# Kernel tuning notes

Hardware: AMD Instinct MI355X
Metric: run time of the kernel (lower is better)

The kernel has to match this reference:

```python
import jax, jax.numpy as jnp
import numpy as np

N_NODES = 50000
N_EDGES = 800000
IN_CH = 128
EDGE_DIM = 16
HID = 64
HEADS = 2
OUT = 64


def _transformer_conv(x, src, dst, edge_attr, Wq, bq, Wk, bk, Wv, bv, We, Ws, bs, H, C):
    # PyG TransformerConv, eval mode, concat=True, root_weight=True, beta=False.
    N = x.shape[0]
    q = (x @ Wq + bq).reshape(N, H, C)
    k = (x @ Wk + bk).reshape(N, H, C)
    v = (x @ Wv + bv).reshape(N, H, C)
    e = (edge_attr @ We).reshape(-1, H, C)          # [E,H,C], lin_edge has no bias
    kj = k[src] + e                                  # gather + edge-aware key
    vj = v[src] + e                                  # gather + edge-aware value
    alpha = jnp.einsum('ehc,ehc->eh', q[dst], kj) / jnp.sqrt(jnp.asarray(C, x.dtype))
    # segment softmax over incoming edges of each target node
    m = jax.ops.segment_max(alpha, dst, num_segments=N)
    m = jnp.where(jnp.isfinite(m), m, jnp.zeros_like(m))
    ex = jnp.exp(alpha - m[dst])
    den = jax.ops.segment_sum(ex, dst, num_segments=N)
    a = ex / (den[dst] + 1e-16)                      # [E,H]
    agg = jax.ops.segment_sum(a[:, :, None] * vj, dst, num_segments=N)  # [N,H,C]
    return agg.reshape(N, H * C) + (x @ Ws + bs)     # concat heads + root skip


def setup_inputs() -> dict:
    key = jax.random.key(0)
    ks = jax.random.split(key, 24)
    s = 0.05
    d1 = HEADS * HID   # 128
    d2 = 1 * OUT       # 64
    inp = {
        'x': jax.random.normal(ks[0], (N_NODES, IN_CH), jnp.float32),
        'edge_index': jax.random.randint(ks[1], (2, N_EDGES), 0, N_NODES, jnp.int32),
        'edge_attr': jax.random.normal(ks[2], (N_EDGES, EDGE_DIM), jnp.float32),
        # layer 1 params
        'Wq1': jax.random.normal(ks[3], (IN_CH, d1), jnp.float32) * s,
        'bq1': jnp.zeros((d1,), jnp.float32),
        'Wk1': jax.random.normal(ks[4], (IN_CH, d1), jnp.float32) * s,
        'bk1': jnp.zeros((d1,), jnp.float32),
        'Wv1': jax.random.normal(ks[5], (IN_CH, d1), jnp.float32) * s,
        'bv1': jnp.zeros((d1,), jnp.float32),
        'We1': jax.random.normal(ks[6], (EDGE_DIM, d1), jnp.float32) * s,
        'Ws1': jax.random.normal(ks[7], (IN_CH, d1), jnp.float32) * s,
        'bs1': jnp.zeros((d1,), jnp.float32),
        # layer 2 params (heads=1)
        'Wq2': jax.random.normal(ks[8], (d1, d2), jnp.float32) * s,
        'bq2': jnp.zeros((d2,), jnp.float32),
        'Wk2': jax.random.normal(ks[9], (d1, d2), jnp.float32) * s,
        'bk2': jnp.zeros((d2,), jnp.float32),
        'Wv2': jax.random.normal(ks[10], (d1, d2), jnp.float32) * s,
        'bv2': jnp.zeros((d2,), jnp.float32),
        'We2': jax.random.normal(ks[11], (EDGE_DIM, d2), jnp.float32) * s,
        'Ws2': jax.random.normal(ks[12], (d1, d2), jnp.float32) * s,
        'bs2': jnp.zeros((d2,), jnp.float32),
    }
    return inp


def reference(x, edge_index, edge_attr,
              Wq1, bq1, Wk1, bk1, Wv1, bv1, We1, Ws1, bs1,
              Wq2, bq2, Wk2, bk2, Wv2, bv2, We2, Ws2, bs2):
    src, dst = edge_index[0], edge_index[1]
    h = _transformer_conv(x, src, dst, edge_attr,
                          Wq1, bq1, Wk1, bk1, Wv1, bv1, We1, Ws1, bs1, HEADS, HID)
    h = jax.nn.relu(h)
    out = _transformer_conv(h, src, dst, edge_attr,
                            Wq2, bq2, Wk2, bk2, Wv2, bv2, We2, Ws2, bs2, 1, OUT)
    return out
```

## Files before the change

### kernel.cpp

```cpp
#include <hip/hip_runtime.h>
#include <hip/hip_bf16.h>

#define NN 50000
#define NE 800000
#define NBKT 196
#define EPB 4096
#define NCB 196

#define PB_BH   NCB
#define PB_PW1  (PB_BH + 32)
#define PB_PW2  (PB_PW1 + 16)
#define PB_PA1  (PB_PW2 + 2)
#define PB_PA2  (PB_PA1 + 1)

#define DB_BKT  NBKT
#define DB_ALL  (DB_BKT + 3125)

typedef __attribute__((ext_vector_type(8))) short bf16x8;
typedef __attribute__((ext_vector_type(4))) float f32x4;

__device__ __forceinline__ float2 bfp(uint32_t u) {
    union { uint32_t i; float f; } lo, hi;
    lo.i = u << 16;
    hi.i = u & 0xffff0000u;
    return make_float2(lo.f, hi.f);
}
__device__ __forceinline__ float bf1(uint16_t u) {
    union { uint32_t i; float f; } x; x.i = ((uint32_t)u) << 16; return x.f;
}
__device__ __forceinline__ float4 bfp4(uint32_t a, uint32_t b) {
    const float2 lo = bfp(a), hi = bfp(b);
    return make_float4(lo.x, lo.y, hi.x, hi.y);
}

template<int M>
__device__ __forceinline__ void pack_w_dev(
    int t, const float* __restrict__ Wq, const float* __restrict__ Wk,
    const float* __restrict__ Wv, const float* __restrict__ Wsk,
    const float* __restrict__ bq, const float* __restrict__ bk,
    const float* __restrict__ bv, const float* __restrict__ bsk,
    __hip_bfloat16* __restrict__ Wp, float* __restrict__ bcat)
{
    constexpr int NFQ = M / 16;
    constexpr int NF_TOT = 4 * NFQ;
    if (t >= 4 * NF_TOT * 64) return;
    const int l  = t & 63;
    const int fg = (t >> 6) % NF_TOT;
    const int s  = t / (64 * NF_TOT);
    const int sec = fg / NFQ;
    const int fl  = fg % NFQ;
    const float* W = sec == 0 ? Wq : sec == 1 ? Wk : sec == 2 ? Wv : Wsk;
    const int col = fl * 16 + (l & 15);
    const int k0  = s * 32 + (l >> 4) * 8;
    __hip_bfloat16 tmp[8];
    #pragma unroll
    for (int j = 0; j < 8; ++j) tmp[j] = __float2bfloat16(W[(size_t)(k0 + j) * M + col]);
    *reinterpret_cast<uint4*>(Wp + ((size_t)(fg * 4 + s) * 64 + l) * 8) =
        *reinterpret_cast<const uint4*>(tmp);
    if (s == 0 && (l >> 4) == 0) {
        const float* B = sec == 0 ? bq : sec == 1 ? bk : sec == 2 ? bv : bsk;
        bcat[fg * 16 + (l & 15)] = B[col];
    }
}

template<int MW, int MO>
__device__ __forceinline__ void pack_wq_dev(
    int t, const float* __restrict__ Wq, const float* __restrict__ We,
    const float* __restrict__ bq,
    __hip_bfloat16* __restrict__ Ap, float* __restrict__ B0)
{
    constexpr int NF = MO / 16;
    if (t >= 4 * NF * 64) return;
    const int l  = t & 63;
    const int fg = (t >> 6) % NF;
    const int s  = t / (64 * NF);
    const int col = fg * 16 + (l & 15);
    const int h = col >> 4;
    const int r = col & 15;
    const int k0 = s * 32 + (l >> 4) * 8;
    __hip_bfloat16 tmp[8];
    #pragma unroll
    for (int jj = 0; jj < 8; ++jj) {
        float acc = 0.f;
        for (int c = 0; c < 64; ++c)
            acc += Wq[(size_t)(k0 + jj) * MW + h * 64 + c] * We[r * MW + h * 64 + c];
        tmp[jj] = __float2bfloat16(acc * 0.125f);
    }
    *reinterpret_cast<uint4*>(Ap + ((size_t)(fg * 4 + s) * 64 + l) * 8) =
        *reinterpret_cast<const uint4*>(tmp);
    if (s == 0 && (l >> 4) == 0) {
        float acc = 0.f;
        for (int c = 0; c < 64; ++c) acc += bq[h * 64 + c] * We[r * MW + h * 64 + c];
        B0[col] = acc * 0.125f;
    }
}

__global__ __launch_bounds__(256)
void prep(const int* __restrict__ dstp, int* __restrict__ blkcnt,
          const float* Wq1, const float* Wk1, const float* Wv1, const float* Ws1,
          const float* bq1, const float* bk1, const float* bv1, const float* bs1,
          const float* We1,
          const float* Wq2, const float* Wk2, const float* Wv2, const float* Ws2,
          const float* bq2, const float* bk2, const float* bv2, const float* bs2,
          const float* We2,
          __hip_bfloat16* Wp1, float* bcat1,
          __hip_bfloat16* Wp2, float* bcat2)
{
    const int b = blockIdx.x;
    const int t = threadIdx.x;
    if (b < PB_BH) {
        __shared__ int bins[NBKT];
        if (t < NBKT) bins[t] = 0;
        __syncthreads();
        const int e0 = b * EPB;
        const int nedge = min(EPB, NE - e0);
        for (int j = 0; j < EPB / 256; ++j) {
            const int idx = t + j * 256;
            if (idx < nedge) atomicAdd(&bins[dstp[e0 + idx] >> 8], 1);
        }
        __syncthreads();
        if (t < NBKT) blkcnt[b * NBKT + t] = bins[t];
    } else if (b < PB_PW1) {
        pack_w_dev<128>((b - PB_BH) * 256 + t, Wq1, Wk1, Wv1, Ws1,
                        bq1, bk1, bv1, bs1, Wp1, bcat1);
    } else if (b < PB_PW2) {
        pack_w_dev<64>((b - PB_PW1) * 256 + t, Wq2, Wk2, Wv2, Ws2,
                       bq2, bk2, bv2, bs2, Wp2, bcat2);
    } else if (b < PB_PA1) {
        pack_wq_dev<128, 32>((b - PB_PW2) * 256 + t, Wq1, We1, bq1,
                             Wp1 + (size_t)32 * 2048, bcat1 + 512);
    } else {
        pack_wq_dev<64, 16>((b - PB_PA1) * 256 + t, Wq2, We2, bq2,
                            Wp2 + (size_t)16 * 2048, bcat2 + 256);
    }
}

__global__ __launch_bounds__(256)
void passC(const int* __restrict__ dstp, const int* __restrict__ srcp,
           const int* __restrict__ blkcnt, int2* __restrict__ ebuf,
           int* __restrict__ bucket_start)
{
    __shared__ int gbase[NBKT];
    __shared__ int lofs0[NBKT];
    __shared__ int lcur[NBKT];
    __shared__ int stmp[256];
    __shared__ int2 buf[EPB];

    const int blk = blockIdx.x;
    const int t = threadIdx.x;

    int partial = 0, total = 0;
    if (t < NBKT) {
        for (int b = 0; b < NCB; ++b) {
            const int v = blkcnt[b * NBKT + t];
            partial += (b < blk) ? v : 0;
            total += v;
        }
    }
    stmp[t] = (t < NBKT) ? total : 0;
    __syncthreads();
    #pragma unroll
    for (int d = 1; d < 256; d <<= 1) {
        const int v = (t >= d) ? stmp[t - d] : 0;
        __syncthreads();
        stmp[t] += v;
        __syncthreads();
    }
    const int bstart = stmp[t] - ((t < NBKT) ? total : 0);
    if (t < NBKT) gbase[t] = bstart + partial;
    if (blk == 0 && t < NBKT) bucket_start[t] = bstart;
    if (blk == 0 && t == NBKT - 1) bucket_start[NBKT] = stmp[t];

    if (t < NBKT) lcur[t] = 0;
    __syncthreads();
    const int e0 = blk * EPB;
    const int nedge = min(EPB, NE - e0);
    for (int j = 0; j < EPB / 256; ++j) {
        const int idx = t + j * 256;
        if (idx < nedge) atomicAdd(&lcur[dstp[e0 + idx] >> 8], 1);
    }
    __syncthreads();
    stmp[t] = (t < NBKT) ? lcur[t] : 0;
    __syncthreads();
    const int own = stmp[t];
    #pragma unroll
    for (int d = 1; d < 256; d <<= 1) {
        const int v = (t >= d) ? stmp[t - d] : 0;
        __syncthreads();
        stmp[t] += v;
        __syncthreads();
    }
    if (t < NBKT) { lofs0[t] = stmp[t] - own; lcur[t] = stmp[t] - own; }
    __syncthreads();

    for (int j = 0; j < EPB / 256; ++j) {
        const int idx = t + j * 256;
        if (idx < nedge) {
            const int e = e0 + idx;
            const int d_ = dstp[e];
            const int bkt = d_ >> 8;
            const int q = atomicAdd(&lcur[bkt], 1);
            buf[q] = make_int2(srcp[e] | ((d_ & 255) << 16), e | (bkt << 20));
        }
    }
    __syncthreads();

    for (int j = 0; j < EPB / 256; ++j) {
        const int q = t + j * 256;
        if (q < nedge) {
            const int2 v = buf[q];
            const int bkt = v.y >> 20;
            ebuf[gbase[bkt] + (q - lofs0[bkt])] = v;
        }
    }
}

template<int M, int MO, bool F32IN>
__device__ __forceinline__
void gemm_dev(int blk, int tid, const void* __restrict__ xin,
              const __hip_bfloat16* __restrict__ Wp,
              const float* __restrict__ bcat,
              __hip_bfloat16* __restrict__ q, __hip_bfloat16* __restrict__ kv,
              __hip_bfloat16* __restrict__ skip, float* __restrict__ wqo)
{
    constexpr int NF_TOT = (4 * M + MO) / 16;
    constexpr int NFW = (NF_TOT + 3) / 4;
    const int wid  = tid >> 6;
    const int l    = tid & 63;
    const int row0 = blk * 16;
    const int rowg = row0 + (l & 15);
    const int kb   = l >> 4;

    f32x4 acc[NFW];
    #pragma unroll
    for (int f = 0; f < NFW; ++f) acc[f] = f32x4{0.f, 0.f, 0.f, 0.f};

    const bf16x8* wp8 = reinterpret_cast<const bf16x8*>(Wp);
    #pragma unroll
    for (int s = 0; s < 4; ++s) {
        bf16x8 a;
        if constexpr (F32IN) {
            const float* xf = (const float*)xin;
            const float4 a0 = *reinterpret_cast<const float4*>(
                xf + (size_t)rowg * 128 + s * 32 + kb * 8);
            const float4 a1 = *reinterpret_cast<const float4*>(
                xf + (size_t)rowg * 128 + s * 32 + kb * 8 + 4);
            union { __hip_bfloat16 h[8]; bf16x8 v; } u;
            u.h[0] = __float2bfloat16(a0.x); u.h[1] = __float2bfloat16(a0.y);
            u.h[2] = __float2bfloat16(a0.z); u.h[3] = __float2bfloat16(a0.w);
            u.h[4] = __float2bfloat16(a1.x); u.h[5] = __float2bfloat16(a1.y);
            u.h[6] = __float2bfloat16(a1.z); u.h[7] = __float2bfloat16(a1.w);
            a = u.v;
        } else {
            const __hip_bfloat16* xb = (const __hip_bfloat16*)xin;
            a = *reinterpret_cast<const bf16x8*>(xb + (size_t)rowg * 128 + s * 32 + kb * 8);
        }
        #pragma unroll
        for (int f = 0; f < NFW; ++f) {
            const int fg = wid + 4 * f;
            if (fg < NF_TOT)
                acc[f] = __builtin_amdgcn_mfma_f32_16x16x32_bf16(
                    a, wp8[(size_t)(fg * 4 + s) * 64 + l], acc[f], 0, 0, 0);
        }
    }

    const int cl = l & 15;
    #pragma unroll
    for (int f = 0; f < NFW; ++f) {
        const int fg = wid + 4 * f;
        if (fg >= NF_TOT) continue;
        const int cg = fg * 16 + cl;
        const float bb = bcat[cg];
        #pragma unroll
        for (int j = 0; j < 4; ++j) {
            const int row = row0 + kb * 4 + j;
            const float val = acc[f][j] + bb;
            if (cg < M) {
                q[(size_t)row * M + cg] = __float2bfloat16(val * 0.125f);
            } else if (cg < 2 * M) {
                const int c = cg - M;
                kv[(size_t)row * 2 * M + (c >> 2) * 8 + (c & 3)] = __float2bfloat16(val);
            } else if (cg < 3 * M) {
                const int c = cg - 2 * M;
                kv[(size_t)row * 2 * M + (c >> 2) * 8 + 4 + (c & 3)] = __float2bfloat16(val);
            } else if (cg < 4 * M) {
                skip[(size_t)row * M + (cg - 3 * M)] = __float2bfloat16(val);
            } else {
                wqo[(size_t)row * MO + (cg - 4 * M)] = val;
            }
        }
    }
}

template<int M, int MO, bool F32IN>
__global__ __launch_bounds__(256)
void gemm_fused(const void* __restrict__ xin,
                const __hip_bfloat16* __restrict__ Wp,
                const float* __restrict__ bcat,
                __hip_bfloat16* __restrict__ q, __hip_bfloat16* __restrict__ kv,
                __hip_bfloat16* __restrict__ skip, float* __restrict__ wqo)
{
    gemm_dev<M, MO, F32IN>(blockIdx.x, threadIdx.x, xin, Wp, bcat, q, kv, skip, wqo);
}

__global__ __launch_bounds__(256)
void passD_mid(const int2* __restrict__ ebuf, const int* __restrict__ bucket_start,
               const float* __restrict__ ea,
               int* __restrict__ off, int* __restrict__ srcs,
               __hip_bfloat16* __restrict__ eap,
               const float* __restrict__ x, const __hip_bfloat16* __restrict__ Wp1,
               const float* __restrict__ bcat1, __hip_bfloat16* __restrict__ q1b,
               __hip_bfloat16* __restrict__ kv1, __hip_bfloat16* __restrict__ sk1b,
               float* __restrict__ wq1)
{
    __shared__ int nbins[256];
    __shared__ int ncur[256];
    __shared__ int stmp[256];

    if (blockIdx.x >= DB_BKT) {
        gemm_dev<128, 32, true>(blockIdx.x - DB_BKT, threadIdx.x, x, Wp1, bcat1,
                                q1b, kv1, sk1b, wq1);
        return;
    }

    const int b = blockIdx.x;
    const int t = threadIdx.x;
    const int bs = bucket_start[b];
    const int be = bucket_start[b + 1];

    nbins[t] = 0;
    __syncthreads();
    for (int i = bs + t; i < be; i += 256)
        atomicAdd(&nbins[(ebuf[i].x >> 16) & 255], 1);
    __syncthreads();

    const int own = nbins[t];
    stmp[t] = own;
    __syncthreads();
    #pragma unroll
    for (int d = 1; d < 256; d <<= 1) {
        const int v = (t >= d) ? stmp[t - d] : 0;
        __syncthreads();
        stmp[t] += v;
        __syncthreads();
    }
    const int excl = stmp[t] - own;
    ncur[t] = excl;
    const int node = b * 256 + t;
    if (node <= NN) off[node] = bs + excl;
    __syncthreads();

    for (int i = bs + t; i < be; i += 256) {
        const int2 v = ebuf[i];
        const int dl = (v.x >> 16) & 255;
        const int p = bs + atomicAdd(&ncur[dl], 1);
        const int srcn = v.x & 0xffff;
        const int e = v.y & 0xfffff;
        srcs[p] = srcn;
        const float4* ea4 = reinterpret_cast<const float4*>(ea) + (size_t)e * 4;
        const float4 a0 = ea4[0], a1 = ea4[1], a2 = ea4[2], a3 = ea4[3];
        const float af[16] = {a0.x,a0.y,a0.z,a0.w, a1.x,a1.y,a1.z,a1.w,
                              a2.x,a2.y,a2.z,a2.w, a3.x,a3.y,a3.z,a3.w};
        __hip_bfloat16 tmp[16];
        #pragma unroll
        for (int r = 0; r < 16; ++r) tmp[r] = __float2bfloat16(af[r]);
        uint4* dp = reinterpret_cast<uint4*>(eap + (size_t)p * 16);
        dp[0] = *reinterpret_cast<const uint4*>(&tmp[0]);
        dp[1] = *reinterpret_cast<const uint4*>(&tmp[8]);
    }
}

__global__ __launch_bounds__(256)
void agg_l1(const int* __restrict__ off, const int* __restrict__ srcs,
            const __hip_bfloat16* __restrict__ eap,
            const float* __restrict__ We,
            const float* __restrict__ wq,
            const __hip_bfloat16* __restrict__ qb,
            const __hip_bfloat16* __restrict__ kv,
            const __hip_bfloat16* __restrict__ skb,
            __hip_bfloat16* __restrict__ hb)
{
    __shared__ float wes[16 * 128];
    for (int i = threadIdx.x; i < 16 * 128; i += 256) wes[i] = We[i];
    __syncthreads();

    const int node = blockIdx.x * 4 + (threadIdx.x >> 6);
    const int lane = threadIdx.x & 63;
    const int hf   = lane >> 5;
    const int hl   = lane & 31;
    const int g    = lane & 15;
    const int ch   = hl * 4;

    const size_t nb = (size_t)node * 128;
    const uint16_t* qu = reinterpret_cast<const uint16_t*>(qb);
    const uint2 qw = *reinterpret_cast<const uint2*>(qu + nb + ch);
    const float4 qv = bfp4(qw.x, qw.y);
    const float wqv = wq[(size_t)node * 32 + (hl >> 4) * 16 + g];
    const uint16_t* kvu = reinterpret_cast<const uint16_t*>(kv);
    const uint16_t* eau = reinterpret_cast<const uint16_t*>(eap);

    float acc0 = 0.f, acc1 = 0.f, acc2 = 0.f, acc3 = 0.f, den = 0.f, eacc = 0.f;
    const int beg = off[node], end = off[node + 1];

    for (int i = beg; i < end; i += 8) {
        const int ii0 = i + hf,     ii1 = i + 2 + hf;
        const int ii2 = i + 4 + hf, ii3 = i + 6 + hf;
        const bool v0 = ii0 < end, v1 = ii1 < end, v2 = ii2 < end, v3 = ii3 < end;
        const int i0 = v0 ? ii0 : beg, i1 = v1 ? ii1 : beg;
        const int i2 = v2 ? ii2 : beg, i3 = v3 ? ii3 : beg;
        const int s0 = srcs[i0], s1 = srcs[i1], s2 = srcs[i2], s3 = srcs[i3];
        const uint4 x0 = *reinterpret_cast<const uint4*>(kvu + (size_t)s0 * 256 + hl * 8);
        const uint4 x1 = *reinterpret_cast<const uint4*>(kvu + (size_t)s1 * 256 + hl * 8);
        const uint4 x2 = *reinterpret_cast<const uint4*>(kvu + (size_t)s2 * 256 + hl * 8);
        const uint4 x3 = *reinterpret_cast<const uint4*>(kvu + (size_t)s3 * 256 + hl * 8);
        const float ea0 = bf1(eau[(size_t)i0 * 16 + g]);
        const float ea1 = bf1(eau[(size_t)i1 * 16 + g]);
        const float ea2 = bf1(eau[(size_t)i2 * 16 + g]);
        const float ea3 = bf1(eau[(size_t)i3 * 16 + g]);
        const float4 k0 = bfp4(x0.x, x0.y), k1 = bfp4(x1.x, x1.y);
        const float4 k2 = bfp4(x2.x, x2.y), k3 = bfp4(x3.x, x3.y);
        float p0 = fmaf(qv.x, k0.x, fmaf(qv.y, k0.y,
                   fmaf(qv.z, k0.z, fmaf(qv.w, k0.w, ea0 * wqv))));
        float p1 = fmaf(qv.x, k1.x, fmaf(qv.y, k1.y,
                   fmaf(qv.z, k1.z, fmaf(qv.w, k1.w, ea1 * wqv))));
        float p2 = fmaf(qv.x, k2.x, fmaf(qv.y, k2.y,
                   fmaf(qv.z, k2.z, fmaf(qv.w, k2.w, ea2 * wqv))));
        float p3 = fmaf(qv.x, k3.x, fmaf(qv.y, k3.y,
                   fmaf(qv.z, k3.z, fmaf(qv.w, k3.w, ea3 * wqv))));
        #pragma unroll
        for (int m = 1; m < 16; m <<= 1) {
            p0 += __shfl_xor(p0, m, 64);
            p1 += __shfl_xor(p1, m, 64);
            p2 += __shfl_xor(p2, m, 64);
            p3 += __shfl_xor(p3, m, 64);
        }
        const float ex0 = v0 ? __expf(p0) : 0.f;
        const float ex1 = v1 ? __expf(p1) : 0.f;
        const float ex2 = v2 ? __expf(p2) : 0.f;
        const float ex3 = v3 ? __expf(p3) : 0.f;
        const float4 w0 = bfp4(x0.z, x0.w), w1 = bfp4(x1.z, x1.w);
        const float4 w2 = bfp4(x2.z, x2.w), w3 = bfp4(x3.z, x3.w);
        acc0 = fmaf(ex0, w0.x, fmaf(ex1, w1.x, fmaf(ex2, w2.x, fmaf(ex3, w3.x, acc0))));
        acc1 = fmaf(ex0, w0.y, fmaf(ex1, w1.y, fmaf(ex2, w2.y, fmaf(ex3, w3.y, acc1))));
        acc2 = fmaf(ex0, w0.z, fmaf(ex1, w1.z, fmaf(ex2, w2.z, fmaf(ex3, w3.z, acc2))));
        acc3 = fmaf(ex0, w0.w, fmaf(ex1, w1.w, fmaf(ex2, w2.w, fmaf(ex3, w3.w, acc3))));
        den += (ex0 + ex1) + (ex2 + ex3);
        eacc = fmaf(ex0, ea0, fmaf(ex1, ea1, fmaf(ex2, ea2, fmaf(ex3, ea3, eacc))));
    }

    acc0 += __shfl_xor(acc0, 32, 64);
    acc1 += __shfl_xor(acc1, 32, 64);
    acc2 += __shfl_xor(acc2, 32, 64);
    acc3 += __shfl_xor(acc3, 32, 64);
    den  += __shfl_xor(den, 32, 64);
    eacc += __shfl_xor(eacc, 32, 64);

    const int gb = lane & 16;
    #pragma unroll
    for (int r = 0; r < 16; ++r) {
        const float er = __shfl(eacc, gb + r, 64);
        const float4 w = *reinterpret_cast<const float4*>(&wes[r * 128 + ch]);
        acc0 = fmaf(er, w.x, acc0);
        acc1 = fmaf(er, w.y, acc1);
        acc2 = fmaf(er, w.z, acc2);
        acc3 = fmaf(er, w.w, acc3);
    }

    if (hf == 0) {
        const float inv = 1.f / (den + 1e-16f);
        const uint16_t* sku = reinterpret_cast<const uint16_t*>(skb);
        const uint2 skw = *reinterpret_cast<const uint2*>(sku + nb + ch);
        const float4 sk = bfp4(skw.x, skw.y);
        __hip_bfloat16 hp[4] = {
            __float2bfloat16(fmaxf(fmaf(acc0, inv, sk.x), 0.f)),
            __float2bfloat16(fmaxf(fmaf(acc1, inv, sk.y), 0.f)),
            __float2bfloat16(fmaxf(fmaf(acc2, inv, sk.z), 0.f)),
            __float2bfloat16(fmaxf(fmaf(acc3, inv, sk.w), 0.f))};
        *reinterpret_cast<uint2*>(hb + nb + ch) = *reinterpret_cast<const uint2*>(hp);
    }
}

__global__ __launch_bounds__(256)
void agg_l2(const int* __restrict__ off, const int* __restrict__ srcs,
            const __hip_bfloat16* __restrict__ eap,
            const float* __restrict__ We,
            const float* __restrict__ wq,
            const __hip_bfloat16* __restrict__ qb,
            const __hip_bfloat16* __restrict__ kv,
            const __hip_bfloat16* __restrict__ skb,
            float* __restrict__ out)
{
    __shared__ float wes[16 * 64];
    for (int i = threadIdx.x; i < 16 * 64; i += 256) wes[i] = We[i];
    __syncthreads();

    const int node = blockIdx.x * 4 + (threadIdx.x >> 6);
    const int lane = threadIdx.x & 63;
    const int grp  = lane >> 4;
    const int g    = lane & 15;
    const int ch   = g * 4;

    const size_t nb = (size_t)node * 64;
    const uint16_t* qu = reinterpret_cast<const uint16_t*>(qb);
    const uint2 qw = *reinterpret_cast<const uint2*>(qu + nb + ch);
    const float4 qv = bfp4(qw.x, qw.y);
    const float wqv = wq[(size_t)node * 16 + g];
    const uint16_t* kvu = reinterpret_cast<const uint16_t*>(kv);
    const uint16_t* eau = reinterpret_cast<const uint16_t*>(eap);

    float acc0 = 0.f, acc1 = 0.f, acc2 = 0.f, acc3 = 0.f, den = 0.f, eacc = 0.f;
    const int beg = off[node], end = off[node + 1];

    for (int i = beg; i < end; i += 8) {
        const int ii0 = i + grp, ii1 = i + 4 + grp;
        const bool v0 = ii0 < end, v1 = ii1 < end;
        const int i0 = v0 ? ii0 : beg, i1 = v1 ? ii1 : beg;
        const int s0 = srcs[i0], s1 = srcs[i1];
        const uint4 x0 = *reinterpret_cast<const uint4*>(kvu + (size_t)s0 * 128 + g * 8);
        const uint4 x1 = *reinterpret_cast<const uint4*>(kvu + (size_t)s1 * 128 + g * 8);
        const float ea0 = bf1(eau[(size_t)i0 * 16 + g]);
        const float ea1 = bf1(eau[(size_t)i1 * 16 + g]);
        const float4 k0 = bfp4(x0.x, x0.y), k1 = bfp4(x1.x, x1.y);
        float p0 = fmaf(qv.x, k0.x, fmaf(qv.y, k0.y,
                   fmaf(qv.z, k0.z, fmaf(qv.w, k0.w, ea0 * wqv))));
        float p1 = fmaf(qv.x, k1.x, fmaf(qv.y, k1.y,
                   fmaf(qv.z, k1.z, fmaf(qv.w, k1.w, ea1 * wqv))));
        #pragma unroll
        for (int m = 1; m < 16; m <<= 1) {
            p0 += __shfl_xor(p0, m, 64);
            p1 += __shfl_xor(p1, m, 64);
        }
        const float ex0 = v0 ? __expf(p0) : 0.f;
        const float ex1 = v1 ? __expf(p1) : 0.f;
        const float4 w0 = bfp4(x0.z, x0.w), w1 = bfp4(x1.z, x1.w);
        acc0 = fmaf(ex0, w0.x, fmaf(ex1, w1.x, acc0));
        acc1 = fmaf(ex0, w0.y, fmaf(ex1, w1.y, acc1));
        acc2 = fmaf(ex0, w0.z, fmaf(ex1, w1.z, acc2));
        acc3 = fmaf(ex0, w0.w, fmaf(ex1, w1.w, acc3));
        den += ex0 + ex1;
        eacc = fmaf(ex0, ea0, fmaf(ex1, ea1, eacc));
    }

    acc0 += __shfl_xor(acc0, 16, 64);  acc0 += __shfl_xor(acc0, 32, 64);
    acc1 += __shfl_xor(acc1, 16, 64);  acc1 += __shfl_xor(acc1, 32, 64);
    acc2 += __shfl_xor(acc2, 16, 64);  acc2 += __shfl_xor(acc2, 32, 64);
    acc3 += __shfl_xor(acc3, 16, 64);  acc3 += __shfl_xor(acc3, 32, 64);
    den  += __shfl_xor(den, 16, 64);   den  += __shfl_xor(den, 32, 64);
    eacc += __shfl_xor(eacc, 16, 64);  eacc += __shfl_xor(eacc, 32, 64);

    #pragma unroll
    for (int r = 0; r < 16; ++r) {
        const float er = __shfl(eacc, r, 64);
        const float4 w = *reinterpret_cast<const float4*>(&wes[r * 64 + ch]);
        acc0 = fmaf(er, w.x, acc0);
        acc1 = fmaf(er, w.y, acc1);
        acc2 = fmaf(er, w.z, acc2);
        acc3 = fmaf(er, w.w, acc3);
    }

    if (lane < 16) {
        const float inv = 1.f / (den + 1e-16f);
        const uint16_t* sku = reinterpret_cast<const uint16_t*>(skb);
        const uint2 skw = *reinterpret_cast<const uint2*>(sku + nb + ch);
        const float4 sk = bfp4(skw.x, skw.y);
        *reinterpret_cast<float4*>(out + nb + ch) =
            make_float4(fmaf(acc0, inv, sk.x), fmaf(acc1, inv, sk.y),
                        fmaf(acc2, inv, sk.z), fmaf(acc3, inv, sk.w));
    }
}

extern "C" void kernel_launch(void* const* d_in, const int* in_sizes, int n_in,
                              void* d_out, int out_size, void* d_ws, size_t ws_size,
                              hipStream_t stream) {
    const float* x     = (const float*)d_in[0];
    const int*   ei    = (const int*)  d_in[1];
    const float* eattr = (const float*)d_in[2];
    const float* Wq1 = (const float*)d_in[3],  *bq1 = (const float*)d_in[4];
    const float* Wk1 = (const float*)d_in[5],  *bk1 = (const float*)d_in[6];
    const float* Wv1 = (const float*)d_in[7],  *bv1 = (const float*)d_in[8];
    const float* We1 = (const float*)d_in[9];
    const float* Ws1 = (const float*)d_in[10], *bs1 = (const float*)d_in[11];
    const float* Wq2 = (const float*)d_in[12], *bq2 = (const float*)d_in[13];
    const float* Wk2 = (const float*)d_in[14], *bk2 = (const float*)d_in[15];
    const float* Wv2 = (const float*)d_in[16], *bv2 = (const float*)d_in[17];
    const float* We2 = (const float*)d_in[18];
    const float* Ws2 = (const float*)d_in[19], *bs2 = (const float*)d_in[20];

    const int* srcp = ei;
    const int* dstp = ei + NE;

    char* base = (char*)d_ws;
    size_t o = 0;
    auto alloc = [&](size_t bytes) -> void* {
        void* p = base + o;
        o = (o + bytes + 511) & ~(size_t)511;
        return p;
    };
    float* wq1   = (float*)alloc((size_t)NN * 32 * 4);
    float* wq2   = (float*)alloc((size_t)NN * 16 * 4);
    float* bcat1 = (float*)alloc(544 * 4);
    float* bcat2 = (float*)alloc(272 * 4);
    int*  blkcnt = (int*)alloc((size_t)NCB * NBKT * 4);
    int2* ebuf   = (int2*)alloc((size_t)NE * 8);
    int*  bstart = (int*)alloc((NBKT + 1) * 4);
    int*  srcs   = (int*)alloc((size_t)NE * 4);
    int*  off    = (int*)alloc((size_t)(NN + 1) * 4);
    __hip_bfloat16* eap  = (__hip_bfloat16*)alloc((size_t)NE * 16 * 2);
    __hip_bfloat16* q1b  = (__hip_bfloat16*)alloc((size_t)NN * 128 * 2);
    __hip_bfloat16* sk1b = (__hip_bfloat16*)alloc((size_t)NN * 128 * 2);
    __hip_bfloat16* hb   = (__hip_bfloat16*)alloc((size_t)NN * 128 * 2);
    __hip_bfloat16* kv1  = (__hip_bfloat16*)alloc((size_t)NN * 256 * 2);
    __hip_bfloat16* Wp1  = (__hip_bfloat16*)alloc((size_t)34 * 2048 * 2);
    __hip_bfloat16* Wp2  = (__hip_bfloat16*)alloc((size_t)17 * 2048 * 2);
    __hip_bfloat16* q2b  = q1b;
    __hip_bfloat16* sk2b = sk1b;
    __hip_bfloat16* kv2  = kv1;

    prep<<<PB_PA2, 256, 0, stream>>>(dstp, blkcnt,
        Wq1, Wk1, Wv1, Ws1, bq1, bk1, bv1, bs1, We1,
        Wq2, Wk2, Wv2, Ws2, bq2, bk2, bv2, bs2, We2,
        Wp1, bcat1, Wp2, bcat2);

    passC<<<NCB, 256, 0, stream>>>(dstp, srcp, blkcnt, ebuf, bstart);

    passD_mid<<<DB_ALL, 256, 0, stream>>>(ebuf, bstart, eattr, off, srcs, eap,
                                          x, Wp1, bcat1, q1b, kv1, sk1b, wq1);

    agg_l1<<<NN / 4, 256, 0, stream>>>(off, srcs, eap, We1, wq1, q1b, kv1, sk1b, hb);

    gemm_fused<64, 16, false><<<NN / 16, 256, 0, stream>>>(
        hb, Wp2, bcat2, q2b, kv2, sk2b, wq2);

    agg_l2<<<NN / 4, 256, 0, stream>>>(off, srcs, eap, We2, wq2, q2b, kv2, sk2b, (float*)d_out);
}
```

Before: 259.7 us.

## Move edge-attr bf16 conversion into bucket scatter and widen blocks to 1024 threads

The bucket scatter pass now scatters each edge straight to its global slot with shared atomics, dropping the shared-memory staging and local prefix scan. It also converts edge attributes to bf16 and writes them to an intermediate array at bucket position. The per-node sort pass then copies 32-byte bf16 rows instead of re-reading 64-byte fp32 rows at random edge indices. Both passes switch to 1024-thread blocks, and the fused GEMM blocks each handle four 16-row tiles. The direct global scatter loses write coalescing and adds a 25.6MB intermediate buffer plus an extra copy.

```diff
diff --git a/kernel.cpp b/kernel.cpp
--- a/kernel.cpp
+++ b/kernel.cpp
@@ -14,7 +14,8 @@
 #define PB_PA2  (PB_PA1 + 1)
 
 #define DB_BKT  NBKT
-#define DB_ALL  (DB_BKT + 3125)
+#define DB_GT   782
+#define DB_ALL  (DB_BKT + DB_GT)
 
 typedef __attribute__((ext_vector_type(8))) short bf16x8;
 typedef __attribute__((ext_vector_type(4))) float f32x4;
@@ -135,16 +136,14 @@
     }
 }
 
-__global__ __launch_bounds__(256)
+__global__ __launch_bounds__(1024)
 void passC(const int* __restrict__ dstp, const int* __restrict__ srcp,
-           const int* __restrict__ blkcnt, int2* __restrict__ ebuf,
+           const float* __restrict__ ea, const int* __restrict__ blkcnt,
+           uint32_t* __restrict__ sidx, __hip_bfloat16* __restrict__ eap1,
            int* __restrict__ bucket_start)
 {
-    __shared__ int gbase[NBKT];
-    __shared__ int lofs0[NBKT];
-    __shared__ int lcur[NBKT];
+    __shared__ int gcur[NBKT];
     __shared__ int stmp[256];
-    __shared__ int2 buf[EPB];
 
     const int blk = blockIdx.x;
     const int t = threadIdx.x;
@@ -157,60 +156,44 @@
             total += v;
         }
     }
-    stmp[t] = (t < NBKT) ? total : 0;
-    __syncthreads();
-    #pragma unroll
+    if (t < 256) stmp[t] = (t < NBKT) ? total : 0;
+    __syncthreads();
     for (int d = 1; d < 256; d <<= 1) {
-        const int v = (t >= d) ? stmp[t - d] : 0;
+        const int v = (t < 256 && t >= d) ? stmp[t - d] : 0;
         __syncthreads();
-        stmp[t] += v;
+        if (t < 256) stmp[t] += v;
         __syncthreads();
     }
-    const int bstart = stmp[t] - ((t < NBKT) ? total : 0);
-    if (t < NBKT) gbase[t] = bstart + partial;
-    if (blk == 0 && t < NBKT) bucket_start[t] = bstart;
-    if (blk == 0 && t == NBKT - 1) bucket_start[NBKT] = stmp[t];
-
-    if (t < NBKT) lcur[t] = 0;
-    __syncthreads();
+    if (t < NBKT) {
+        const int bstart = stmp[t] - total;
+        gcur[t] = bstart + partial;
+        if (blk == 0) {
+            bucket_start[t] = bstart;
+            if (t == NBKT - 1) bucket_start[NBKT] = stmp[t];
+        }
+    }
+    __syncthreads();
+
     const int e0 = blk * EPB;
     const int nedge = min(EPB, NE - e0);
-    for (int j = 0; j < EPB / 256; ++j) {
-        const int idx = t + j * 256;
-        if (idx < nedge) atomicAdd(&lcur[dstp[e0 + idx] >> 8], 1);
-    }
-    __syncthreads();
-    stmp[t] = (t < NBKT) ? lcur[t] : 0;
-    __syncthreads();
-    const int own = stmp[t];
-    #pragma unroll
-    for (int d = 1; d < 256; d <<= 1) {
-        const int v = (t >= d) ? stmp[t - d] : 0;
-        __syncthreads();
-        stmp[t] += v;
-        __syncthreads();
-    }
-    if (t < NBKT) { lofs0[t] = stmp[t] - own; lcur[t] = stmp[t] - own; }
-    __syncthreads();
-
-    for (int j = 0; j < EPB / 256; ++j) {
-        const int idx = t + j * 256;
+    for (int j = 0; j < EPB / 1024; ++j) {
+        const int idx = t + j * 1024;
         if (idx < nedge) {
             const int e = e0 + idx;
             const int d_ = dstp[e];
             const int bkt = d_ >> 8;
-            const int q = atomicAdd(&lcur[bkt], 1);
-            buf[q] = make_int2(srcp[e] | ((d_ & 255) << 16), e | (bkt << 20));
-        }
-    }
-    __syncthreads();
-
-    for (int j = 0; j < EPB / 256; ++j) {
-        const int q = t + j * 256;
-        if (q < nedge) {
-            const int2 v = buf[q];
-            const int bkt = v.y >> 20;
-            ebuf[gbase[bkt] + (q - lofs0[bkt])] = v;
+            const int p = atomicAdd(&gcur[bkt], 1);
+            sidx[p] = (uint32_t)srcp[e] | ((uint32_t)(d_ & 255) << 16);
+            const float4* ea4 = reinterpret_cast<const float4*>(ea) + (size_t)e * 4;
+            const float4 a0 = ea4[0], a1 = ea4[1], a2 = ea4[2], a3 = ea4[3];
+            const float af[16] = {a0.x,a0.y,a0.z,a0.w, a1.x,a1.y,a1.z,a1.w,
+                                  a2.x,a2.y,a2.z,a2.w, a3.x,a3.y,a3.z,a3.w};
+            __hip_bfloat16 tmp[16];
+            #pragma unroll
+            for (int r = 0; r < 16; ++r) tmp[r] = __float2bfloat16(af[r]);
+            uint4* dp = reinterpret_cast<uint4*>(eap1 + (size_t)p * 16);
+            dp[0] = *reinterpret_cast<const uint4*>(&tmp[0]);
+            dp[1] = *reinterpret_cast<const uint4*>(&tmp[8]);
         }
     }
 }
@@ -303,9 +286,9 @@
     gemm_dev<M, MO, F32IN>(blockIdx.x, threadIdx.x, xin, Wp, bcat, q, kv, skip, wqo);
 }
 
-__global__ __launch_bounds__(256)
-void passD_mid(const int2* __restrict__ ebuf, const int* __restrict__ bucket_start,
-               const float* __restrict__ ea,
+__global__ __launch_bounds__(1024)
+void passD_mid(const uint32_t* __restrict__ sidx, const __hip_bfloat16* __restrict__ eap1,
+               const int* __restrict__ bucket_start,
                int* __restrict__ off, int* __restrict__ srcs,
                __hip_bfloat16* __restrict__ eap,
                const float* __restrict__ x, const __hip_bfloat16* __restrict__ Wp1,
@@ -318,8 +301,10 @@
     __shared__ int stmp[256];
 
     if (blockIdx.x >= DB_BKT) {
-        gemm_dev<128, 32, true>(blockIdx.x - DB_BKT, threadIdx.x, x, Wp1, bcat1,
-                                q1b, kv1, sk1b, wq1);
+        const int tile = (blockIdx.x - DB_BKT) * 4 + (threadIdx.x >> 8);
+        if (tile < 3125)
+            gemm_dev<128, 32, true>(tile, threadIdx.x & 255, x, Wp1, bcat1,
+                                    q1b, kv1, sk1b, wq1);
         return;
     }
 
@@ -328,45 +313,38 @@
     const int bs = bucket_start[b];
     const int be = bucket_start[b + 1];
 
-    nbins[t] = 0;
-    __syncthreads();
-    for (int i = bs + t; i < be; i += 256)
-        atomicAdd(&nbins[(ebuf[i].x >> 16) & 255], 1);
-    __syncthreads();
-
-    const int own = nbins[t];
-    stmp[t] = own;
-    __syncthreads();
-    #pragma unroll
+    if (t < 256) nbins[t] = 0;
+    __syncthreads();
+    for (int i = bs + t; i < be; i += 1024)
+        atomicAdd(&nbins[(sidx[i] >> 16) & 255], 1);
+    __syncthreads();
+
+    if (t < 256) stmp[t] = nbins[t];
+    __syncthreads();
     for (int d = 1; d < 256; d <<= 1) {
-        const int v = (t >= d) ? stmp[t - d] : 0;
+        const int v = (t < 256 && t >= d) ? stmp[t - d] : 0;
         __syncthreads();
-        stmp[t] += v;
+        if (t < 256) stmp[t] += v;
         __syncthreads();
     }
-    const int excl = stmp[t] - own;
-    ncur[t] = excl;
-    const int node = b * 256 + t;
-    if (node <= NN) off[node] = bs + excl;
-    __syncthreads();
-
-    for (int i = bs + t; i < be; i += 256) {
-        const int2 v = ebuf[i];
-        const int dl = (v.x >> 16) & 255;
+    if (t < 256) {
+        const int own = nbins[t];
+        const int excl = stmp[t] - own;
+        ncur[t] = excl;
+        const int node = b * 256 + t;
+        if (node <= NN) off[node] = bs + excl;
+    }
+    __syncthreads();
+
+    for (int i = bs + t; i < be; i += 1024) {
+        const uint32_t v = sidx[i];
+        const int dl = (v >> 16) & 255;
         const int p = bs + atomicAdd(&ncur[dl], 1);
-        const int srcn = v.x & 0xffff;
-        const int e = v.y & 0xfffff;
-        srcs[p] = srcn;
-        const float4* ea4 = reinterpret_cast<const float4*>(ea) + (size_t)e * 4;
-        const float4 a0 = ea4[0], a1 = ea4[1], a2 = ea4[2], a3 = ea4[3];
-        const float af[16] = {a0.x,a0.y,a0.z,a0.w, a1.x,a1.y,a1.z,a1.w,
-                              a2.x,a2.y,a2.z,a2.w, a3.x,a3.y,a3.z,a3.w};
-        __hip_bfloat16 tmp[16];
-        #pragma unroll
-        for (int r = 0; r < 16; ++r) tmp[r] = __float2bfloat16(af[r]);
+        srcs[p] = (int)(v & 0xffffu);
+        const uint4* sp = reinterpret_cast<const uint4*>(eap1 + (size_t)i * 16);
         uint4* dp = reinterpret_cast<uint4*>(eap + (size_t)p * 16);
-        dp[0] = *reinterpret_cast<const uint4*>(&tmp[0]);
-        dp[1] = *reinterpret_cast<const uint4*>(&tmp[8]);
+        dp[0] = sp[0];
+        dp[1] = sp[1];
     }
 }
 
@@ -601,10 +579,11 @@
     float* bcat1 = (float*)alloc(544 * 4);
     float* bcat2 = (float*)alloc(272 * 4);
     int*  blkcnt = (int*)alloc((size_t)NCB * NBKT * 4);
-    int2* ebuf   = (int2*)alloc((size_t)NE * 8);
+    uint32_t* sidx = (uint32_t*)alloc((size_t)NE * 4);
     int*  bstart = (int*)alloc((NBKT + 1) * 4);
     int*  srcs   = (int*)alloc((size_t)NE * 4);
     int*  off    = (int*)alloc((size_t)(NN + 1) * 4);
+    __hip_bfloat16* eap1 = (__hip_bfloat16*)alloc((size_t)NE * 16 * 2);
     __hip_bfloat16* eap  = (__hip_bfloat16*)alloc((size_t)NE * 16 * 2);
     __hip_bfloat16* q1b  = (__hip_bfloat16*)alloc((size_t)NN * 128 * 2);
     __hip_bfloat16* sk1b = (__hip_bfloat16*)alloc((size_t)NN * 128 * 2);
@@ -621,10 +600,10 @@
         Wq2, Wk2, Wv2, Ws2, bq2, bk2, bv2, bs2, We2,
         Wp1, bcat1, Wp2, bcat2);
 
-    passC<<<NCB, 256, 0, stream>>>(dstp, srcp, blkcnt, ebuf, bstart);
-
-    passD_mid<<<DB_ALL, 256, 0, stream>>>(ebuf, bstart, eattr, off, srcs, eap,
-                                          x, Wp1, bcat1, q1b, kv1, sk1b, wq1);
+    passC<<<NCB, 1024, 0, stream>>>(dstp, srcp, eattr, blkcnt, sidx, eap1, bstart);
+
+    passD_mid<<<DB_ALL, 1024, 0, stream>>>(sidx, eap1, bstart, off, srcs, eap,
+                                           x, Wp1, bcat1, q1b, kv1, sk1b, wq1);
 
     agg_l1<<<NN / 4, 256, 0, stream>>>(off, srcs, eap, We1, wq1, q1b, kv1, sk1b, hb);
 
```

New measurement: 265.1 us. 2.1% more time.
